# Kernel tuning notes

Hardware: AMD Instinct MI355X
Metric: run time of the kernel (lower is better)

Reference implementation:

```python
import jax, jax.numpy as jnp
import numpy as np

B, T, D, S = 64, 577, 768, 577  # batch, seq, hidden, v-out (=seq of e)


def setup_inputs() -> dict:
    key = jax.random.key(0)
    ks = jax.random.split(key, 8)
    sc = 1.0 / np.sqrt(D)
    return {
        "b": jax.random.normal(ks[0], (B, T, D), jnp.float32),
        "e": jax.random.normal(ks[1], (B, T, D), jnp.float32),
        "Wq": jax.random.normal(ks[2], (D, D), jnp.float32) * sc,
        "bq": jnp.zeros((D,), jnp.float32),
        "Wk": jax.random.normal(ks[3], (D, D), jnp.float32) * sc,
        "bk": jnp.zeros((D,), jnp.float32),
        "Wv": jax.random.normal(ks[4], (S, D), jnp.float32) * sc,
        "bv": jnp.zeros((S,), jnp.float32),
    }


def reference(b, e, Wq, bq, Wk, bk, Wv, bv):
    # Dropout layers are identity in eval mode.
    q = b @ Wq.T + bq                      # [B,T,D]
    k = e @ Wk.T + bk                      # [B,S,D]
    v = b @ Wv.T + bv                      # [B,T,S]
    # tanh(Q K^T) @ V^T : [B,T,S] @ [B,S,T] -> [B,T,T]
    attn = jnp.tanh(jnp.einsum("btd,bsd->bts", q, k))
    out = jnp.einsum("bts,bus->btu", attn, v)
    return out  # squeeze is a no-op for B>1
```

## Files before the change

kernel.cpp:

```cpp
#include <hip/hip_runtime.h>
#include <hip/hip_fp16.h>


typedef _Float16 f16x8 __attribute__((ext_vector_type(8)));
typedef _Float16 f16x4 __attribute__((ext_vector_type(4)));
typedef float f32x4 __attribute__((ext_vector_type(4)));

__global__ void cvt8_kernel(const float* __restrict__ src, _Float16* __restrict__ dst,
                            long long n8) {
    long long i = blockIdx.x * (long long)blockDim.x + threadIdx.x;
    const long long stride = gridDim.x * (long long)blockDim.x;
    for (; i < n8; i += stride) {
        const float4 f0 = ((const float4*)src)[2 * i];
        const float4 f1 = ((const float4*)src)[2 * i + 1];
        f16x8 h;
        h[0] = (_Float16)f0.x; h[1] = (_Float16)f0.y; h[2] = (_Float16)f0.z; h[3] = (_Float16)f0.w;
        h[4] = (_Float16)f1.x; h[5] = (_Float16)f1.y; h[6] = (_Float16)f1.z; h[7] = (_Float16)f1.w;
        ((f16x8*)dst)[i] = h;
    }
}

__global__ void cvtT2_kernel(const float* __restrict__ s0, _Float16* __restrict__ d0,
                             const float* __restrict__ s1, _Float16* __restrict__ d1) {
    __shared__ float t[32][33];
    const float* src = blockIdx.z ? s1 : s0;
    _Float16* dst = blockIdx.z ? d1 : d0;
    const int bx = blockIdx.x, by = blockIdx.y;
    const int tx = threadIdx.x & 31, ty = threadIdx.x >> 5;
#pragma unroll
    for (int k = 0; k < 4; ++k) {
        const int r = ty + 8 * k;
        t[r][tx] = src[(size_t)(by * 32 + r) * 768 + bx * 32 + tx];
    }
    __syncthreads();
#pragma unroll
    for (int k = 0; k < 4; ++k) {
        const int r = ty + 8 * k;
        dst[(size_t)(bx * 32 + r) * 768 + by * 32 + tx] = (_Float16)t[tx][r];
    }
}

__global__ void prep_kernel(const _Float16* __restrict__ WqT, const _Float16* __restrict__ WkT,
                            const float* __restrict__ bq, const float* __restrict__ bk,
                            const float* __restrict__ bv,
                            float* __restrict__ w2f, _Float16* __restrict__ Mt_aug,
                            float* __restrict__ bias_mg) {
    const int wid = blockIdx.x * 4 + (threadIdx.x >> 6);
    const int lane = threadIdx.x & 63;
    if (wid < 768) {
        float s = 0.f;
        for (int k = 0; k < 12; ++k) s += (float)WqT[(size_t)wid * 768 + lane + 64 * k] * bk[lane + 64 * k];
        for (int o = 32; o; o >>= 1) s += __shfl_xor(s, o);
        if (lane == 0) Mt_aug[(size_t)768 * 768 + wid] = (_Float16)s;
    } else if (wid < 1536) {
        const int n = wid - 768;
        float s = 0.f;
        for (int k = 0; k < 12; ++k) s += (float)WkT[(size_t)n * 768 + lane + 64 * k] * bq[lane + 64 * k];
        for (int o = 32; o; o >>= 1) s += __shfl_xor(s, o);
        if (lane == 0) w2f[n] = s;
    } else if (wid == 1536) {
        float s = 0.f;
        for (int k = 0; k < 12; ++k) s += bq[lane + 64 * k] * bk[lane + 64 * k];
        for (int o = 32; o; o >>= 1) s += __shfl_xor(s, o);
        if (lane < 32) {
            float v = 0.f;
            if (lane == 0) v = s;
            if (lane == 1) v = 1.f;
            bias_mg[768 + lane] = v;
        }
    } else if (wid < 1560) {
        const int i = (wid - 1537) * 64 + lane;
        if (i < 768) bias_mg[i] = 0.f;
        else {
            const int j = i + 32;
            if (j < 1408) bias_mg[j] = (j < 1377) ? bv[j - 800] : 0.f;
        }
    } else if (wid < 1591) {
        const int r = 769 + (wid - 1560);
        for (int k = 0; k < 12; ++k) Mt_aug[(size_t)r * 768 + lane + 64 * k] = (_Float16)0.f;
    }
}

__global__ void cvt_e_aug_kernel(const float* __restrict__ e, const float* __restrict__ w2f,
                                 _Float16* __restrict__ dst, int rows) {
    const int wpb = blockDim.x >> 6;
    int wid = blockIdx.x * wpb + (threadIdx.x >> 6);
    const int nw = gridDim.x * wpb;
    const int lane = threadIdx.x & 63;
    for (int s = wid; s < rows; s += nw) {
        const float4* er = (const float4*)(e + (size_t)s * 768);
        _Float16* dr = dst + (size_t)s * 800;
        float dot = 0.f;
#pragma unroll
        for (int k = 0; k < 3; ++k) {
            const int idx = lane + 64 * k;
            const float4 v = er[idx];
            const float4 w = ((const float4*)w2f)[idx];
            dot += v.x * w.x + v.y * w.y + v.z * w.z + v.w * w.w;
            f16x4 h;
            h[0] = (_Float16)v.x; h[1] = (_Float16)v.y;
            h[2] = (_Float16)v.z; h[3] = (_Float16)v.w;
            *(f16x4*)(dr + 4 * idx) = h;
        }
        for (int o = 32; o; o >>= 1) dot += __shfl_xor(dot, o);
        if (lane < 32) {
            _Float16 v = (_Float16)0.f;
            if (lane == 0) v = (_Float16)1.f;
            if (lane == 1) v = (_Float16)dot;
            dr[768 + lane] = v;
        }
    }
}

__device__ __forceinline__ void gload16(const _Float16* g, _Float16* l) {
    __builtin_amdgcn_global_load_lds(
        (const __attribute__((address_space(1))) unsigned int*)(g),
        (__attribute__((address_space(3))) unsigned int*)(l),
        16, 0, 0);
}

template<bool TANH, bool OUT_F16, bool BIAS, int MODE>
__global__ __launch_bounds__(256)
void gemm_nt_f16(const _Float16* __restrict__ A, const _Float16* __restrict__ Bt,
                 const float* __restrict__ bias, void* __restrict__ Cp,
                 int M, int Nreal, int Nstore, int K,
                 int lda, int ldb, int ldc, int nTileN, int nTiles,
                 long long sA, long long sB, long long sC)
{
    __shared__ __align__(16) _Float16 lds[3 * 8192];

    int bid = blockIdx.x;
    int z, tm, tn;
    if (MODE == 0) {
        const int nwg = gridDim.x;
        const int q8 = nwg >> 3, r8 = nwg & 7;
        const int xcd = bid & 7, loc = bid >> 3;
        bid = (xcd < r8 ? xcd * (q8 + 1) : r8 * (q8 + 1) + (xcd - r8) * q8) + loc;
        z = 0;
        tm = bid / nTileN; tn = bid - tm * nTileN;
    } else {
        const int xcd = bid & 7, idx = bid >> 3;
        const int g = idx / nTiles, tile = idx - g * nTiles;
        z = g * 8 + xcd;
        tm = tile / nTileN; tn = tile - tm * nTileN;
    }
    const int m0 = tm << 7, n0 = tn << 7;

    const _Float16* Az = A + (size_t)z * sA;
    const _Float16* Bz = Bt + (size_t)z * sB;

    const int tid = threadIdx.x;
    const int lane = tid & 63;
    const int wid = tid >> 6;
    const int wm = wid >> 1, wn = wid & 1;

    const int r0 = tid >> 2;
    const int c0 = (((tid & 3) ^ ((tid >> 3) & 3)) << 3);
    const int rA0 = (m0 + r0      < M ? m0 + r0      : M - 1);
    const int rA1 = (m0 + r0 + 64 < M ? m0 + r0 + 64 : M - 1);
    const int rB0 = (n0 + r0      < Nreal ? n0 + r0      : Nreal - 1);
    const int rB1 = (n0 + r0 + 64 < Nreal ? n0 + r0 + 64 : Nreal - 1);
    const _Float16* pA0 = Az + (size_t)rA0 * lda + c0;
    const _Float16* pA1 = Az + (size_t)rA1 * lda + c0;
    const _Float16* pB0 = Bz + (size_t)rB0 * ldb + c0;
    const _Float16* pB1 = Bz + (size_t)rB1 * ldb + c0;

    const int o0 = tid * 8, o1 = (tid + 256) * 8;

    const int rr = lane & 15;
    const int hh = lane >> 4;
    const int sw = (rr >> 1) & 3;
    const int fAo = ((wm * 64 + rr) * 4 + (hh ^ sw)) * 8;
    const int fBo = ((wn * 64 + rr) * 4 + (hh ^ sw)) * 8;

    const f32x4 z4 = {0.f, 0.f, 0.f, 0.f};
    f32x4 acc[4][4];
#pragma unroll
    for (int i = 0; i < 4; ++i)
#pragma unroll
        for (int j = 0; j < 4; ++j) acc[i][j] = z4;

    const int nt = K >> 5;

#define STAGE(si, kt)                                              \
    do {                                                           \
        _Float16* base_ = lds + (si) * 8192;                       \
        const int ko_ = (kt) << 5;                                 \
        gload16(pA0 + ko_, base_ + o0);                            \
        gload16(pA1 + ko_, base_ + o1);                            \
        gload16(pB0 + ko_, base_ + 4096 + o0);                     \
        gload16(pB1 + ko_, base_ + 4096 + o1);                     \
    } while (0)

#define COMPUTE(si)                                                            \
    do {                                                                       \
        const _Float16* cA_ = lds + (si) * 8192;                               \
        const _Float16* cB_ = cA_ + 4096;                                      \
        f16x8 a_[4], b_[4];                                                    \
        _Pragma("unroll")                                                      \
        for (int mi = 0; mi < 4; ++mi) a_[mi] = *(const f16x8*)(cA_ + fAo + mi * 512); \
        _Pragma("unroll")                                                      \
        for (int ni = 0; ni < 4; ++ni) b_[ni] = *(const f16x8*)(cB_ + fBo + ni * 512); \
        _Pragma("unroll")                                                      \
        for (int mi = 0; mi < 4; ++mi)                                         \
            _Pragma("unroll")                                                  \
            for (int ni = 0; ni < 4; ++ni)                                     \
                acc[mi][ni] = __builtin_amdgcn_mfma_f32_16x16x32_f16(          \
                    a_[mi], b_[ni], acc[mi][ni], 0, 0, 0);                     \
    } while (0)

    STAGE(0, 0);
    STAGE(1, 1);

    for (int j = 0; j < nt - 1; ++j) {
        asm volatile("s_waitcnt vmcnt(4)" ::: "memory");
        __builtin_amdgcn_s_barrier();
        __builtin_amdgcn_sched_barrier(0);
        if (j + 2 < nt) STAGE((j + 2) % 3, j + 2);
        COMPUTE(j % 3);
    }
    asm volatile("s_waitcnt vmcnt(0)" ::: "memory");
    __builtin_amdgcn_s_barrier();
    __builtin_amdgcn_sched_barrier(0);
    COMPUTE((nt - 1) % 3);

#undef STAGE
#undef COMPUTE

    const int cr0 = (lane >> 4) << 2;
    const int cc = lane & 15;
    float*    Cf = (float*)Cp    + (size_t)z * sC;
    _Float16* Ch = (_Float16*)Cp + (size_t)z * sC;
#pragma unroll
    for (int mi = 0; mi < 4; ++mi) {
#pragma unroll
        for (int ni = 0; ni < 4; ++ni) {
            const int gc = n0 + wn * 64 + ni * 16 + cc;
            if (gc >= Nstore) continue;
            const bool real = gc < Nreal;
            float bb = 0.f;
            if (BIAS) bb = real ? bias[gc] : 0.f;
#pragma unroll
            for (int r = 0; r < 4; ++r) {
                const int gr = m0 + wm * 64 + mi * 16 + cr0 + r;
                if (gr >= M) continue;
                float x = real ? (acc[mi][ni][r] + bb) : 0.f;
                if (TANH) x = tanhf(x);
                if (OUT_F16) Ch[(size_t)gr * ldc + gc] = (_Float16)x;
                else         Cf[(size_t)gr * ldc + gc] = x;
            }
        }
    }
}

extern "C" void kernel_launch(void* const* d_in, const int* in_sizes, int n_in,
                              void* d_out, int out_size, void* d_ws, size_t ws_size,
                              hipStream_t stream)
{
    const float* b  = (const float*)d_in[0];
    const float* e  = (const float*)d_in[1];
    const float* Wq = (const float*)d_in[2];
    const float* bq = (const float*)d_in[3];
    const float* Wk = (const float*)d_in[4];
    const float* bk = (const float*)d_in[5];
    const float* Wv = (const float*)d_in[6];
    const float* bv = (const float*)d_in[7];
    float* out = (float*)d_out;

    const int BT = 36928, T = 577, S = 577, Sp = 608, Kb = 800;
    const int Nmg = 1408;

    _Float16* WqT_h  = (_Float16*)d_ws;
    _Float16* WkT_h  = WqT_h + 589824;
    _Float16* Mt_aug = WkT_h + 589824;
    _Float16* Wv_h   = Mt_aug + 614400;
    float*    bias_mg = (float*)(Wv_h + 443136);
    float*    w2f     = (float*)((_Float16*)bias_mg + 2816);
    _Float16* S1    = (_Float16*)w2f + 1536;
    _Float16* S_big = S1 + (size_t)BT * Kb;
    _Float16* S4    = S_big + (size_t)BT * Nmg;

    cvtT2_kernel<<<dim3(24, 24, 2), 256, 0, stream>>>(Wq, WqT_h, Wk, WkT_h);
    cvt8_kernel<<<217, 256, 0, stream>>>(Wv, Wv_h, 55392);
    prep_kernel<<<398, 256, 0, stream>>>(WqT_h, WkT_h, bq, bk, bv, w2f, Mt_aug, bias_mg);
    gemm_nt_f16<false, true, false, 0><<<dim3(36, 1, 1), 256, 0, stream>>>(
        WkT_h, WqT_h, nullptr, Mt_aug, 768, 768, 768, 768, 768, 768, 768, 6, 0, 0, 0, 0);

    cvt8_kernel<<<2048, 256, 0, stream>>>(b, S1, 3545088);
    gemm_nt_f16<false, true, true, 0><<<dim3(3179, 1, 1), 256, 0, stream>>>(
        S1, Mt_aug, bias_mg, S_big, BT, 1377, Nmg, 768, 768, 768, Nmg, 11, 0, 0, 0, 0);
    cvt_e_aug_kernel<<<2048, 256, 0, stream>>>(e, w2f, S1, BT);
    gemm_nt_f16<true, true, false, 1><<<dim3(1600, 1, 1), 256, 0, stream>>>(
        S_big, S1, nullptr, S4, T, S, Sp, Kb, Nmg, Kb, Sp, 5, 25,
        (long long)T * Nmg, (long long)T * Kb, (long long)T * Sp);
    gemm_nt_f16<false, false, false, 1><<<dim3(1600, 1, 1), 256, 0, stream>>>(
        S4, S_big + 800, nullptr, out, T, T, T, Sp, Sp, Nmg, T, 5, 25,
        (long long)T * Sp, (long long)T * Nmg, (long long)T * T);
}
```

Measured before the change: 354.7 us.

## Add BK=64 double-buffered GEMM for projection and tanh-score GEMMs

Adds a second GEMM kernel that stages 64-wide K slices per iteration with two LDS buffers, instead of 32-wide slices with three buffers. The wide projection GEMM and the tanh score GEMM now use it. This halves the number of barrier and wait rounds per tile and does twice as many MFMAs per sync. To make K a multiple of 64, the augmented e buffer is padded from 800 to 832 columns, and the extra columns are zero-filled. In exchange it does slightly more work on the padded K, uses 64KB of LDS per block (which may limit occupancy), and waits for all loads to finish each step, which leaves less load latency overlapped.

```diff
diff --git a/kernel.cpp b/kernel.cpp
--- a/kernel.cpp
+++ b/kernel.cpp
@@ -89,7 +89,7 @@
     const int lane = threadIdx.x & 63;
     for (int s = wid; s < rows; s += nw) {
         const float4* er = (const float4*)(e + (size_t)s * 768);
-        _Float16* dr = dst + (size_t)s * 800;
+        _Float16* dr = dst + (size_t)s * 832;
         float dot = 0.f;
 #pragma unroll
         for (int k = 0; k < 3; ++k) {
@@ -103,7 +103,7 @@
             *(f16x4*)(dr + 4 * idx) = h;
         }
         for (int o = 32; o; o >>= 1) dot += __shfl_xor(dot, o);
-        if (lane < 32) {
+        {
             _Float16 v = (_Float16)0.f;
             if (lane == 0) v = (_Float16)1.f;
             if (lane == 1) v = (_Float16)dot;
@@ -117,6 +117,143 @@
         (const __attribute__((address_space(1))) unsigned int*)(g),
         (__attribute__((address_space(3))) unsigned int*)(l),
         16, 0, 0);
+}
+
+#define GEMM_SETUP(TILE_SHIFT)                                                  \
+    int bid = blockIdx.x;                                                       \
+    int z, tm, tn;                                                              \
+    if (MODE == 0) {                                                            \
+        const int nwg = gridDim.x;                                              \
+        const int q8 = nwg >> 3, r8 = nwg & 7;                                  \
+        const int xcd = bid & 7, loc = bid >> 3;                                \
+        bid = (xcd < r8 ? xcd * (q8 + 1) : r8 * (q8 + 1) + (xcd - r8) * q8) + loc; \
+        z = 0;                                                                  \
+        tm = bid / nTileN; tn = bid - tm * nTileN;                              \
+    } else {                                                                    \
+        const int xcd = bid & 7, idx = bid >> 3;                                \
+        const int g = idx / nTiles, tile = idx - g * nTiles;                    \
+        z = g * 8 + xcd;                                                        \
+        tm = tile / nTileN; tn = tile - tm * nTileN;                            \
+    }                                                                           \
+    const int m0 = tm << 7, n0 = tn << 7;                                       \
+    const _Float16* Az = A + (size_t)z * sA;                                    \
+    const _Float16* Bz = Bt + (size_t)z * sB;                                   \
+    const int tid = threadIdx.x;                                                \
+    const int lane = tid & 63;                                                  \
+    const int wid = tid >> 6;                                                   \
+    const int wm = wid >> 1, wn = wid & 1;                                      \
+    const int r0 = tid >> 2;                                                    \
+    const int c0 = (((tid & 3) ^ ((tid >> 3) & 3)) << 3);                       \
+    const int rA0 = (m0 + r0      < M ? m0 + r0      : M - 1);                  \
+    const int rA1 = (m0 + r0 + 64 < M ? m0 + r0 + 64 : M - 1);                  \
+    const int rB0 = (n0 + r0      < Nreal ? n0 + r0      : Nreal - 1);          \
+    const int rB1 = (n0 + r0 + 64 < Nreal ? n0 + r0 + 64 : Nreal - 1);          \
+    const _Float16* pA0 = Az + (size_t)rA0 * lda + c0;                          \
+    const _Float16* pA1 = Az + (size_t)rA1 * lda + c0;                          \
+    const _Float16* pB0 = Bz + (size_t)rB0 * ldb + c0;                          \
+    const _Float16* pB1 = Bz + (size_t)rB1 * ldb + c0;                          \
+    const int o0 = tid * 8, o1 = (tid + 256) * 8;                               \
+    const int rr = lane & 15;                                                   \
+    const int hh = lane >> 4;                                                   \
+    const int sw = (rr >> 1) & 3;                                               \
+    const int fAo = ((wm * 64 + rr) * 4 + (hh ^ sw)) * 8;                       \
+    const int fBo = ((wn * 64 + rr) * 4 + (hh ^ sw)) * 8;                       \
+    const f32x4 z4 = {0.f, 0.f, 0.f, 0.f};                                      \
+    f32x4 acc[4][4];                                                            \
+    _Pragma("unroll")                                                           \
+    for (int i = 0; i < 4; ++i)                                                 \
+        _Pragma("unroll")                                                       \
+        for (int j = 0; j < 4; ++j) acc[i][j] = z4;
+
+#define GEMM_EPILOGUE                                                           \
+    const int cr0 = (lane >> 4) << 2;                                           \
+    const int cc = lane & 15;                                                   \
+    float*    Cf = (float*)Cp    + (size_t)z * sC;                              \
+    _Float16* Ch = (_Float16*)Cp + (size_t)z * sC;                              \
+    _Pragma("unroll")                                                           \
+    for (int mi = 0; mi < 4; ++mi) {                                            \
+        _Pragma("unroll")                                                       \
+        for (int ni = 0; ni < 4; ++ni) {                                        \
+            const int gc = n0 + wn * 64 + ni * 16 + cc;                         \
+            if (gc >= Nstore) continue;                                         \
+            const bool real = gc < Nreal;                                       \
+            float bb = 0.f;                                                     \
+            if (BIAS) bb = real ? bias[gc] : 0.f;                               \
+            _Pragma("unroll")                                                   \
+            for (int r = 0; r < 4; ++r) {                                       \
+                const int gr = m0 + wm * 64 + mi * 16 + cr0 + r;                \
+                if (gr >= M) continue;                                          \
+                float x = real ? (acc[mi][ni][r] + bb) : 0.f;                   \
+                if (TANH) x = tanhf(x);                                         \
+                if (OUT_F16) Ch[(size_t)gr * ldc + gc] = (_Float16)x;           \
+                else         Cf[(size_t)gr * ldc + gc] = x;                     \
+            }                                                                   \
+        }                                                                       \
+    }
+
+template<bool TANH, bool OUT_F16, bool BIAS, int MODE>
+__global__ __launch_bounds__(256)
+void gemm64_nt(const _Float16* __restrict__ A, const _Float16* __restrict__ Bt,
+               const float* __restrict__ bias, void* __restrict__ Cp,
+               int M, int Nreal, int Nstore, int K,
+               int lda, int ldb, int ldc, int nTileN, int nTiles,
+               long long sA, long long sB, long long sC)
+{
+    __shared__ __align__(16) _Float16 lds[2 * 16384];
+
+    GEMM_SETUP(7)
+
+    const int nt = K >> 6;
+
+#define STAGE64(s, kt)                                                 \
+    do {                                                               \
+        _Float16* base_ = lds + (s) * 16384;                           \
+        const int ko_ = (kt) << 6;                                     \
+        gload16(pA0 + ko_,      base_ + o0);                           \
+        gload16(pA1 + ko_,      base_ + o1);                           \
+        gload16(pA0 + ko_ + 32, base_ + 4096 + o0);                    \
+        gload16(pA1 + ko_ + 32, base_ + 4096 + o1);                    \
+        gload16(pB0 + ko_,      base_ + 8192 + o0);                    \
+        gload16(pB1 + ko_,      base_ + 8192 + o1);                    \
+        gload16(pB0 + ko_ + 32, base_ + 12288 + o0);                   \
+        gload16(pB1 + ko_ + 32, base_ + 12288 + o1);                   \
+    } while (0)
+
+#define COMPUTE64(s)                                                            \
+    do {                                                                        \
+        const _Float16* bA_ = lds + (s) * 16384;                                \
+        const _Float16* bB_ = bA_ + 8192;                                       \
+        _Pragma("unroll")                                                       \
+        for (int sub = 0; sub < 2; ++sub) {                                     \
+            f16x8 a_[4], b_[4];                                                 \
+            _Pragma("unroll")                                                   \
+            for (int mi = 0; mi < 4; ++mi)                                      \
+                a_[mi] = *(const f16x8*)(bA_ + sub * 4096 + fAo + mi * 512);    \
+            _Pragma("unroll")                                                   \
+            for (int ni = 0; ni < 4; ++ni)                                      \
+                b_[ni] = *(const f16x8*)(bB_ + sub * 4096 + fBo + ni * 512);    \
+            _Pragma("unroll")                                                   \
+            for (int mi = 0; mi < 4; ++mi)                                      \
+                _Pragma("unroll")                                               \
+                for (int ni = 0; ni < 4; ++ni)                                  \
+                    acc[mi][ni] = __builtin_amdgcn_mfma_f32_16x16x32_f16(       \
+                        a_[mi], b_[ni], acc[mi][ni], 0, 0, 0);                  \
+        }                                                                       \
+    } while (0)
+
+    STAGE64(0, 0);
+    for (int j = 0; j < nt; ++j) {
+        asm volatile("s_waitcnt vmcnt(0)" ::: "memory");
+        __builtin_amdgcn_s_barrier();
+        __builtin_amdgcn_sched_barrier(0);
+        if (j + 1 < nt) STAGE64((j + 1) & 1, j + 1);
+        COMPUTE64(j & 1);
+    }
+
+#undef STAGE64
+#undef COMPUTE64
+
+    GEMM_EPILOGUE
 }
 
 template<bool TANH, bool OUT_F16, bool BIAS, int MODE>
@@ -129,56 +266,7 @@
 {
     __shared__ __align__(16) _Float16 lds[3 * 8192];
 
-    int bid = blockIdx.x;
-    int z, tm, tn;
-    if (MODE == 0) {
-        const int nwg = gridDim.x;
-        const int q8 = nwg >> 3, r8 = nwg & 7;
-        const int xcd = bid & 7, loc = bid >> 3;
-        bid = (xcd < r8 ? xcd * (q8 + 1) : r8 * (q8 + 1) + (xcd - r8) * q8) + loc;
-        z = 0;
-        tm = bid / nTileN; tn = bid - tm * nTileN;
-    } else {
-        const int xcd = bid & 7, idx = bid >> 3;
-        const int g = idx / nTiles, tile = idx - g * nTiles;
-        z = g * 8 + xcd;
-        tm = tile / nTileN; tn = tile - tm * nTileN;
-    }
-    const int m0 = tm << 7, n0 = tn << 7;
-
-    const _Float16* Az = A + (size_t)z * sA;
-    const _Float16* Bz = Bt + (size_t)z * sB;
-
-    const int tid = threadIdx.x;
-    const int lane = tid & 63;
-    const int wid = tid >> 6;
-    const int wm = wid >> 1, wn = wid & 1;
-
-    const int r0 = tid >> 2;
-    const int c0 = (((tid & 3) ^ ((tid >> 3) & 3)) << 3);
-    const int rA0 = (m0 + r0      < M ? m0 + r0      : M - 1);
-    const int rA1 = (m0 + r0 + 64 < M ? m0 + r0 + 64 : M - 1);
-    const int rB0 = (n0 + r0      < Nreal ? n0 + r0      : Nreal - 1);
-    const int rB1 = (n0 + r0 + 64 < Nreal ? n0 + r0 + 64 : Nreal - 1);
-    const _Float16* pA0 = Az + (size_t)rA0 * lda + c0;
-    const _Float16* pA1 = Az + (size_t)rA1 * lda + c0;
-    const _Float16* pB0 = Bz + (size_t)rB0 * ldb + c0;
-    const _Float16* pB1 = Bz + (size_t)rB1 * ldb + c0;
-
-    const int o0 = tid * 8, o1 = (tid + 256) * 8;
-
-    const int rr = lane & 15;
-    const int hh = lane >> 4;
-    const int sw = (rr >> 1) & 3;
-    const int fAo = ((wm * 64 + rr) * 4 + (hh ^ sw)) * 8;
-    const int fBo = ((wn * 64 + rr) * 4 + (hh ^ sw)) * 8;
-
-    const f32x4 z4 = {0.f, 0.f, 0.f, 0.f};
-    f32x4 acc[4][4];
-#pragma unroll
-    for (int i = 0; i < 4; ++i)
-#pragma unroll
-        for (int j = 0; j < 4; ++j) acc[i][j] = z4;
+    GEMM_SETUP(7)
 
     const int nt = K >> 5;
 
@@ -227,30 +315,7 @@
 #undef STAGE
 #undef COMPUTE
 
-    const int cr0 = (lane >> 4) << 2;
-    const int cc = lane & 15;
-    float*    Cf = (float*)Cp    + (size_t)z * sC;
-    _Float16* Ch = (_Float16*)Cp + (size_t)z * sC;
-#pragma unroll
-    for (int mi = 0; mi < 4; ++mi) {
-#pragma unroll
-        for (int ni = 0; ni < 4; ++ni) {
-            const int gc = n0 + wn * 64 + ni * 16 + cc;
-            if (gc >= Nstore) continue;
-            const bool real = gc < Nreal;
-            float bb = 0.f;
-            if (BIAS) bb = real ? bias[gc] : 0.f;
-#pragma unroll
-            for (int r = 0; r < 4; ++r) {
-                const int gr = m0 + wm * 64 + mi * 16 + cr0 + r;
-                if (gr >= M) continue;
-                float x = real ? (acc[mi][ni][r] + bb) : 0.f;
-                if (TANH) x = tanhf(x);
-                if (OUT_F16) Ch[(size_t)gr * ldc + gc] = (_Float16)x;
-                else         Cf[(size_t)gr * ldc + gc] = x;
-            }
-        }
-    }
+    GEMM_EPILOGUE
 }
 
 extern "C" void kernel_launch(void* const* d_in, const int* in_sizes, int n_in,
@@ -267,7 +332,8 @@
     const float* bv = (const float*)d_in[7];
     float* out = (float*)d_out;
 
-    const int BT = 36928, T = 577, S = 577, Sp = 608, Kb = 800;
+    const int BT = 36928, T = 577, S = 577, Sp = 608;
+    const int Ke = 832;
     const int Nmg = 1408;
 
     _Float16* WqT_h  = (_Float16*)d_ws;
@@ -277,7 +343,7 @@
     float*    bias_mg = (float*)(Wv_h + 443136);
     float*    w2f     = (float*)((_Float16*)bias_mg + 2816);
     _Float16* S1    = (_Float16*)w2f + 1536;
-    _Float16* S_big = S1 + (size_t)BT * Kb;
+    _Float16* S_big = S1 + (size_t)BT * Ke;
     _Float16* S4    = S_big + (size_t)BT * Nmg;
 
     cvtT2_kernel<<<dim3(24, 24, 2), 256, 0, stream>>>(Wq, WqT_h, Wk, WkT_h);
@@ -287,12 +353,12 @@
         WkT_h, WqT_h, nullptr, Mt_aug, 768, 768, 768, 768, 768, 768, 768, 6, 0, 0, 0, 0);
 
     cvt8_kernel<<<2048, 256, 0, stream>>>(b, S1, 3545088);
-    gemm_nt_f16<false, true, true, 0><<<dim3(3179, 1, 1), 256, 0, stream>>>(
+    gemm64_nt<false, true, true, 0><<<dim3(3179, 1, 1), 256, 0, stream>>>(
         S1, Mt_aug, bias_mg, S_big, BT, 1377, Nmg, 768, 768, 768, Nmg, 11, 0, 0, 0, 0);
     cvt_e_aug_kernel<<<2048, 256, 0, stream>>>(e, w2f, S1, BT);
-    gemm_nt_f16<true, true, false, 1><<<dim3(1600, 1, 1), 256, 0, stream>>>(
-        S_big, S1, nullptr, S4, T, S, Sp, Kb, Nmg, Kb, Sp, 5, 25,
-        (long long)T * Nmg, (long long)T * Kb, (long long)T * Sp);
+    gemm64_nt<true, true, false, 1><<<dim3(1600, 1, 1), 256, 0, stream>>>(
+        S_big, S1, nullptr, S4, T, S, Sp, Ke, Nmg, Ke, Sp, 5, 25,
+        (long long)T * Nmg, (long long)T * Ke, (long long)T * Sp);
     gemm_nt_f16<false, false, false, 1><<<dim3(1600, 1, 1), 256, 0, stream>>>(
         S4, S_big + 800, nullptr, out, T, T, T, Sp, Sp, Nmg, T, 5, 25,
         (long long)T * Sp, (long long)T * Nmg, (long long)T * T);
```

After: 385.2 us. 1.09x slower.

## Use 256x256-tile 512-thread pipelined GEMM for the large projection

Applied to the files above, without the earlier changes.

Adds a dedicated 256x256 tile GEMM kernel with 8 waves, a double-buffered LDS pipeline using direct global-to-LDS loads, interleaved staging and MFMA phases with priority hints, and swizzled LDS layout. It replaces the smaller-tile generic GEMM for the big b-projection (BT x 1377 x 768). The goal is more data reuse per tile and better overlap of loads with MFMA work. In exchange it uses 128KB of LDS and many accumulator registers, which limits occupancy, and it leaves more wasted work on partial edge tiles.

```diff
diff --git a/kernel.cpp b/kernel.cpp
--- a/kernel.cpp
+++ b/kernel.cpp
@@ -119,6 +119,145 @@
         16, 0, 0);
 }
 
+__global__ __launch_bounds__(512, 2)
+void gemm256(const _Float16* __restrict__ A, const _Float16* __restrict__ Bt,
+             const float* __restrict__ bias, _Float16* __restrict__ C,
+             int M, int Nreal, int Nstore, int K,
+             int lda, int ldb, int ldc, int nTileN)
+{
+    __shared__ __align__(16) _Float16 lds[65536];
+
+    int bid = blockIdx.x;
+    {
+        const int nwg = gridDim.x;
+        const int q8 = nwg >> 3, r8 = nwg & 7;
+        const int xcd = bid & 7, loc = bid >> 3;
+        bid = (xcd < r8 ? xcd * (q8 + 1) : r8 * (q8 + 1) + (xcd - r8) * q8) + loc;
+    }
+    const int tm = bid / nTileN, tn = bid - tm * nTileN;
+    const int m0 = tm << 8, n0 = tn << 8;
+
+    const int tid = threadIdx.x;
+    const int lane = tid & 63;
+    const int wid = tid >> 6;
+    const int wm = wid >> 2;
+    const int wn = wid & 3;
+    const int nhB = wn >> 1;
+
+    const int srow = tid >> 2;
+    const int scol = (((tid & 3) ^ ((tid >> 3) & 3)) << 3);
+    int ra0 = m0 + srow;        if (ra0 >= M) ra0 = M - 1;
+    int ra1 = m0 + 128 + srow;  if (ra1 >= M) ra1 = M - 1;
+    int rb0 = n0 + srow;        if (rb0 >= Nreal) rb0 = Nreal - 1;
+    int rb1 = n0 + 128 + srow;  if (rb1 >= Nreal) rb1 = Nreal - 1;
+    const _Float16* pA[2] = { A + (size_t)ra0 * lda + scol, A + (size_t)ra1 * lda + scol };
+    const _Float16* pB[2] = { Bt + (size_t)rb0 * ldb + scol, Bt + (size_t)rb1 * ldb + scol };
+
+    const int rr = lane & 15;
+    const int hh = lane >> 4;
+    const int sw = (rr >> 1) & 3;
+    const int fA0 = (rr * 4 + (hh ^ sw)) * 8;
+    const int fB0 = (wn & 1) * 2048 + fA0;
+
+#define SA(p, mh, kh, kt) \
+    gload16(pA[mh] + ((kt) << 6) + ((kh) << 5), lds + ((p) * 4 + (mh) * 2 + (kh)) * 4096 + tid * 8)
+#define SB(p, nh, kh, kt) \
+    gload16(pB[nh] + ((kt) << 6) + ((kh) << 5), lds + 32768 + ((p) * 4 + (nh) * 2 + (kh)) * 4096 + tid * 8)
+#define RA(p, kh, mi) (*(const f16x8*)(lds + ((p) * 4 + wm * 2 + (kh)) * 4096 + fA0 + (mi) * 512))
+#define RB(p, kh, nj) (*(const f16x8*)(lds + 32768 + ((p) * 4 + nhB * 2 + (kh)) * 4096 + fB0 + (nj) * 512))
+
+    const f32x4 z4 = {0.f, 0.f, 0.f, 0.f};
+    f32x4 acc[8][4];
+#pragma unroll
+    for (int i = 0; i < 8; ++i)
+#pragma unroll
+        for (int j = 0; j < 4; ++j) acc[i][j] = z4;
+
+    const int nt = K >> 6;
+
+#define MMA(mq, a00, a01, a10, a11)                                                  \
+    do {                                                                             \
+        _Pragma("unroll")                                                            \
+        for (int nj = 0; nj < 4; ++nj) {                                             \
+            acc[2*(mq)][nj]   = __builtin_amdgcn_mfma_f32_16x16x32_f16(a00, bf[nj][0], acc[2*(mq)][nj], 0, 0, 0);   \
+            acc[2*(mq)][nj]   = __builtin_amdgcn_mfma_f32_16x16x32_f16(a01, bf[nj][1], acc[2*(mq)][nj], 0, 0, 0);   \
+            acc[2*(mq)+1][nj] = __builtin_amdgcn_mfma_f32_16x16x32_f16(a10, bf[nj][0], acc[2*(mq)+1][nj], 0, 0, 0); \
+            acc[2*(mq)+1][nj] = __builtin_amdgcn_mfma_f32_16x16x32_f16(a11, bf[nj][1], acc[2*(mq)+1][nj], 0, 0, 0); \
+        }                                                                            \
+    } while (0)
+
+#define PHASE(p, mq, BLOAD, STAGEOPS, WAITOP)                                        \
+    do {                                                                             \
+        f16x8 a00 = RA(p, 0, 2*(mq)),   a01 = RA(p, 1, 2*(mq));                      \
+        f16x8 a10 = RA(p, 0, 2*(mq)+1), a11 = RA(p, 1, 2*(mq)+1);                    \
+        if (BLOAD) {                                                                 \
+            _Pragma("unroll")                                                        \
+            for (int nj = 0; nj < 4; ++nj) {                                         \
+                bf[nj][0] = RB(p, 0, nj);                                            \
+                bf[nj][1] = RB(p, 1, nj);                                            \
+            }                                                                        \
+        }                                                                            \
+        STAGEOPS;                                                                    \
+        WAITOP;                                                                      \
+        __builtin_amdgcn_s_barrier();                                                \
+        asm volatile("s_waitcnt lgkmcnt(0)" ::: "memory");                           \
+        __builtin_amdgcn_sched_barrier(0);                                           \
+        __builtin_amdgcn_s_setprio(1);                                               \
+        MMA(mq, a00, a01, a10, a11);                                                 \
+        __builtin_amdgcn_s_setprio(0);                                               \
+        __builtin_amdgcn_s_barrier();                                                \
+    } while (0)
+
+    SA(0,0,0,0); SA(0,0,1,0); SA(0,1,0,0); SA(0,1,1,0);
+    SB(0,0,0,0); SB(0,0,1,0); SB(0,1,0,0); SB(0,1,1,0);
+    SB(1,0,0,1); SB(1,0,1,1); SB(1,1,0,1); SB(1,1,1,1);
+    asm volatile("s_waitcnt vmcnt(4)" ::: "memory");
+    __builtin_amdgcn_s_barrier();
+
+    f16x8 bf[4][2];
+    for (int t = 0; t < nt; t += 2) {
+        const bool more = (t + 2 < nt);
+        PHASE(0, 0, true,  { SA(1,0,0,t+1); SA(1,0,1,t+1); }, );
+        PHASE(0, 1, false, { SA(1,1,0,t+1); SA(1,1,1,t+1); }, );
+        PHASE(0, 2, false, { if (more) { SB(0,0,0,t+2); SB(0,0,1,t+2); } }, );
+        PHASE(0, 3, false, { if (more) { SB(0,1,0,t+2); SB(0,1,1,t+2); } },
+              { if (more) asm volatile("s_waitcnt vmcnt(4)" ::: "memory");
+                else      asm volatile("s_waitcnt vmcnt(0)" ::: "memory"); });
+        PHASE(1, 0, true,  { if (more) { SA(0,0,0,t+2); SA(0,0,1,t+2); } }, );
+        PHASE(1, 1, false, { if (more) { SA(0,1,0,t+2); SA(0,1,1,t+2); } }, );
+        PHASE(1, 2, false, { if (more) { SB(1,0,0,t+3); SB(1,0,1,t+3); } }, );
+        PHASE(1, 3, false, { if (more) { SB(1,1,0,t+3); SB(1,1,1,t+3); } },
+              { if (more) asm volatile("s_waitcnt vmcnt(4)" ::: "memory"); });
+    }
+
+#undef SA
+#undef SB
+#undef RA
+#undef RB
+#undef MMA
+#undef PHASE
+
+    const int cr0 = (lane >> 4) << 2;
+    const int cc = lane & 15;
+#pragma unroll
+    for (int mi = 0; mi < 8; ++mi) {
+#pragma unroll
+        for (int nj = 0; nj < 4; ++nj) {
+            const int gc = n0 + wn * 64 + nj * 16 + cc;
+            if (gc >= Nstore) continue;
+            const bool real = gc < Nreal;
+            const float bb = real ? bias[gc] : 0.f;
+#pragma unroll
+            for (int r = 0; r < 4; ++r) {
+                const int gr = m0 + wm * 128 + mi * 16 + cr0 + r;
+                if (gr >= M) continue;
+                const float x = real ? (acc[mi][nj][r] + bb) : 0.f;
+                C[(size_t)gr * ldc + gc] = (_Float16)x;
+            }
+        }
+    }
+}
+
 template<bool TANH, bool OUT_F16, bool BIAS, int MODE>
 __global__ __launch_bounds__(256)
 void gemm_nt_f16(const _Float16* __restrict__ A, const _Float16* __restrict__ Bt,
@@ -287,8 +426,8 @@
         WkT_h, WqT_h, nullptr, Mt_aug, 768, 768, 768, 768, 768, 768, 768, 6, 0, 0, 0, 0);
 
     cvt8_kernel<<<2048, 256, 0, stream>>>(b, S1, 3545088);
-    gemm_nt_f16<false, true, true, 0><<<dim3(3179, 1, 1), 256, 0, stream>>>(
-        S1, Mt_aug, bias_mg, S_big, BT, 1377, Nmg, 768, 768, 768, Nmg, 11, 0, 0, 0, 0);
+    gemm256<<<dim3(870, 1, 1), 512, 0, stream>>>(
+        S1, Mt_aug, bias_mg, S_big, BT, 1377, Nmg, 768, 768, 768, Nmg, 6);
     cvt_e_aug_kernel<<<2048, 256, 0, stream>>>(e, w2f, S1, BT);
     gemm_nt_f16<true, true, false, 1><<<dim3(1600, 1, 1), 256, 0, stream>>>(
         S_big, S1, nullptr, S4, T, S, Sp, Kb, Nmg, Kb, Sp, 5, 25,
```

New measurement: 377.5 us. 1.06x slower.
